# Kernel optimization log

Measured on AMD Instinct MI355X. Metric: run time of the kernel, lower is better.

## Reference

```python
import jax, jax.numpy as jnp
import numpy as np

EPS = 1e-5

def _point_batch_norm(x, gamma, beta):
    # BatchNorm1d over channel dim of (B, N, C): stats over (B, N), biased var (training mode)
    mu = jnp.mean(x, axis=(0, 1))
    var = jnp.var(x, axis=(0, 1))
    return (x - mu) * jax.lax.rsqrt(var + EPS) * gamma + beta

def setup_inputs() -> dict:
    key = jax.random.key(0)
    ks = jax.random.split(key, 10)
    B, M, N, K = 4, 16384, 32768, 16
    C, Cs, O = 64, 64, 64
    curr_coords = jax.random.normal(ks[0], (B, M, 3), jnp.float32)
    curr_feat = jax.random.normal(ks[1], (B, M, C), jnp.float32)
    skip_coords = jax.random.normal(ks[2], (B, N, 3), jnp.float32)
    skip_feat = jax.random.normal(ks[3], (B, N, Cs), jnp.float32)
    upsampling_idxs = jax.random.randint(ks[4], (B, N, K), 0, M, jnp.int64)
    s1 = 1.0 / np.sqrt(C)
    s2 = 1.0 / np.sqrt(Cs)
    W1 = jax.random.uniform(ks[5], (C, O), jnp.float32, -s1, s1)
    b1 = jax.random.uniform(ks[6], (O,), jnp.float32, -s1, s1)
    W2 = jax.random.uniform(ks[7], (Cs, O), jnp.float32, -s2, s2)
    b2 = jax.random.uniform(ks[8], (O,), jnp.float32, -s2, s2)
    g1 = jnp.ones((O,), jnp.float32); beta1 = jnp.zeros((O,), jnp.float32)
    g2 = jnp.ones((O,), jnp.float32); beta2 = jnp.zeros((O,), jnp.float32)
    return {
        "curr_coords": curr_coords, "curr_feat": curr_feat,
        "skip_coords": skip_coords, "skip_feat": skip_feat,
        "upsampling_idxs": upsampling_idxs,
        "W1": W1, "b1": b1, "g1": g1, "beta1": beta1,
        "W2": W2, "b2": b2, "g2": g2, "beta2": beta2,
    }

def reference(curr_coords, curr_feat, skip_coords, skip_feat, upsampling_idxs,
              W1, b1, g1, beta1, W2, b2, g2, beta2):
    # Gather K-NN neighbor features per skip point: (B, N, K, C), then max over K
    gathered = jax.vmap(lambda f, i: f[i])(curr_feat, upsampling_idxs)
    pooled = jnp.max(gathered, axis=2)  # (B, N, C)
    # proj: Linear -> PointBatchNorm -> ReLU
    h = jax.nn.relu(_point_batch_norm(pooled @ W1 + b1, g1, beta1))
    # proj_skip on skip features
    hs = jax.nn.relu(_point_batch_norm(skip_feat @ W2 + b2, g2, beta2))
    return jnp.concatenate([skip_coords, h, hs], axis=-1)  # (B, N, 3 + 2*O)
```

## Files before the change

### kernel.cpp

```cpp
#include <hip/hip_runtime.h>
#include <hip/hip_bf16.h>

#define BB 4
#define MM 16384
#define NN 32768
#define KK 16
#define ROWS (BB * NN)
#define OUTW 131
#define RPW 32
#define A_BLOCKS (ROWS / (RPW * 4))

__global__ __launch_bounds__(256) void k_pool_proj(
    const float* __restrict__ cf, const int* __restrict__ idxs,
    const float* __restrict__ scoord,
    const float* __restrict__ W1, const float* __restrict__ b1,
    float* __restrict__ out, float* __restrict__ acc)
{
    __shared__ float pool[4][64];
    __shared__ float lsum[64], lsq[64];
    const int lane = threadIdx.x & 63;
    const int wv   = threadIdx.x >> 6;
    if (threadIdx.x < 64) { lsum[threadIdx.x] = 0.f; lsq[threadIdx.x] = 0.f; }
    __syncthreads();

    const int xcd   = blockIdx.x & 7;
    const int batch = xcd >> 1;
    const int blkIB = ((blockIdx.x >> 3) << 1) | (xcd & 1);
    const int gw    = blkIB * 4 + wv;
    const int rbase = (batch << 15) + gw * RPW;

    float w[64];
#pragma unroll
    for (int c = 0; c < 64; ++c) w[c] = W1[c * 64 + lane];
    const float bias = b1[lane];

    float psum = 0.f, psq = 0.f;
    for (int r0 = 0; r0 < RPW; ++r0) {
        const int r = rbase + r0;
        int mi = 0;
        if (lane < KK) mi = idxs[r * KK + lane];
        float pmax = -3.402823466e38f;
#pragma unroll
        for (int k = 0; k < KK; ++k) {
            const int m = __shfl(mi, k);
            pmax = fmaxf(pmax, cf[(((batch << 14) + m) << 6) + lane]);
        }
        pool[wv][lane] = pmax;
        __builtin_amdgcn_wave_barrier();

        const float4* t4 = (const float4*)(&pool[wv][0]);
        float y = bias;
#pragma unroll
        for (int c4 = 0; c4 < 16; ++c4) {
            const float4 p = t4[c4];
            y = fmaf(p.x, w[c4 * 4 + 0], y);
            y = fmaf(p.y, w[c4 * 4 + 1], y);
            y = fmaf(p.z, w[c4 * 4 + 2], y);
            y = fmaf(p.w, w[c4 * 4 + 3], y);
        }
        __builtin_amdgcn_wave_barrier();

        const size_t ob = (size_t)r * OUTW;
        out[ob + 3 + lane] = y;
        if (lane < 3) out[ob + lane] = scoord[r * 3 + lane];
        psum += y; psq += y * y;
    }
    atomicAdd(&lsum[lane], psum);
    atomicAdd(&lsq[lane], psq);
    __syncthreads();
    if (threadIdx.x < 64) {
        atomicAdd(&acc[threadIdx.x],      lsum[threadIdx.x]);
        atomicAdd(&acc[64 + threadIdx.x], lsq[threadIdx.x]);
    }
}

__global__ __launch_bounds__(256) void k_skip_proj(
    const float* __restrict__ sf,
    const float* __restrict__ W2, const float* __restrict__ b2,
    float* __restrict__ out, float* __restrict__ acc)
{
    __shared__ float srow[4][64];
    __shared__ float lsum[64], lsq[64];
    const int lane = threadIdx.x & 63;
    const int wv   = threadIdx.x >> 6;
    if (threadIdx.x < 64) { lsum[threadIdx.x] = 0.f; lsq[threadIdx.x] = 0.f; }
    __syncthreads();

    float w[64];
#pragma unroll
    for (int c = 0; c < 64; ++c) w[c] = W2[c * 64 + lane];
    const float bias = b2[lane];

    float psum = 0.f, psq = 0.f;
    const int gw = blockIdx.x * 4 + wv;
    for (int r0 = 0; r0 < RPW; ++r0) {
        const int r = gw * RPW + r0;
        srow[wv][lane] = sf[(size_t)r * 64 + lane];
        __builtin_amdgcn_wave_barrier();

        const float4* t4 = (const float4*)(&srow[wv][0]);
        float y = bias;
#pragma unroll
        for (int c4 = 0; c4 < 16; ++c4) {
            const float4 p = t4[c4];
            y = fmaf(p.x, w[c4 * 4 + 0], y);
            y = fmaf(p.y, w[c4 * 4 + 1], y);
            y = fmaf(p.z, w[c4 * 4 + 2], y);
            y = fmaf(p.w, w[c4 * 4 + 3], y);
        }
        __builtin_amdgcn_wave_barrier();

        out[(size_t)r * OUTW + 67 + lane] = y;
        psum += y; psq += y * y;
    }
    atomicAdd(&lsum[lane], psum);
    atomicAdd(&lsq[lane], psq);
    __syncthreads();
    if (threadIdx.x < 64) {
        atomicAdd(&acc[128 + threadIdx.x], lsum[threadIdx.x]);
        atomicAdd(&acc[192 + threadIdx.x], lsq[threadIdx.x]);
    }
}

__global__ void k_stats(float* __restrict__ ws,
                        const float* __restrict__ g1, const float* __restrict__ be1,
                        const float* __restrict__ g2, const float* __restrict__ be2)
{
    const int o = threadIdx.x;
    const float inv = 1.0f / (float)ROWS;
    float m1 = ws[o] * inv;
    float v1 = ws[64 + o] * inv - m1 * m1;
    float a1 = g1[o] * rsqrtf(v1 + 1e-5f);
    ws[256 + o] = a1;
    ws[384 + o] = be1[o] - m1 * a1;
    float m2 = ws[128 + o] * inv;
    float v2 = ws[192 + o] * inv - m2 * m2;
    float a2 = g2[o] * rsqrtf(v2 + 1e-5f);
    ws[256 + 64 + o] = a2;
    ws[384 + 64 + o] = be2[o] - m2 * a2;
}

__global__ __launch_bounds__(256) void k_finalize(float* __restrict__ out,
                                                  const float* __restrict__ ws)
{
    const size_t T  = (size_t)gridDim.x * blockDim.x;
    const size_t t0 = (size_t)blockIdx.x * blockDim.x + threadIdx.x;
#pragma unroll
    for (int i = 0; i < 4; ++i) {
        const size_t e = t0 + (size_t)i * T;
        const size_t r = e >> 7;
        const int    j = (int)(e & 127);
        const size_t ad = r * OUTW + 3 + j;
        const float v = out[ad];
        out[ad] = fmaxf(fmaf(v, ws[256 + j], ws[384 + j]), 0.f);
    }
}

extern "C" void kernel_launch(void* const* d_in, const int* in_sizes, int n_in,
                              void* d_out, int out_size, void* d_ws, size_t ws_size,
                              hipStream_t stream)
{
    const float* cf     = (const float*)d_in[1];
    const float* scoord = (const float*)d_in[2];
    const float* sf     = (const float*)d_in[3];
    const int*   idxs   = (const int*)  d_in[4];
    const float* W1     = (const float*)d_in[5];
    const float* b1     = (const float*)d_in[6];
    const float* g1     = (const float*)d_in[7];
    const float* be1    = (const float*)d_in[8];
    const float* W2     = (const float*)d_in[9];
    const float* b2     = (const float*)d_in[10];
    const float* g2     = (const float*)d_in[11];
    const float* be2    = (const float*)d_in[12];
    float* out = (float*)d_out;
    float* ws  = (float*)d_ws;

    hipMemsetAsync(ws, 0, 256 * sizeof(float), stream);
    k_pool_proj<<<A_BLOCKS, 256, 0, stream>>>(cf, idxs, scoord, W1, b1, out, ws);
    k_skip_proj<<<A_BLOCKS, 256, 0, stream>>>(sf, W2, b2, out, ws);
    k_stats<<<1, 64, 0, stream>>>(ws, g1, be1, g2, be2);
    k_finalize<<<16384, 256, 0, stream>>>(out, ws);
}
```

Measured before the change: 293.2 us.

## Process four rows per iteration with batched gathers and slotted stat atomics

Both projection kernels now handle four rows per loop iteration. The pool kernel issues 64 independent gather loads per iteration to raise memory-level parallelism, and the skip kernel loads four rows with a single float4 load. Rows per wave drop to 16, which doubles the block count, and launch bounds request 5 blocks per CU. Global stat atomics are spread across 16 slots that k_stats then reduces, which cuts atomic contention. The costs are more register pressure from four accumulators and a larger workspace memset.

```diff
diff --git a/kernel.cpp b/kernel.cpp
--- a/kernel.cpp
+++ b/kernel.cpp
@@ -7,16 +7,19 @@
 #define KK 16
 #define ROWS (BB * NN)
 #define OUTW 131
-#define RPW 32
+#define RPW 16
 #define A_BLOCKS (ROWS / (RPW * 4))
-
-__global__ __launch_bounds__(256) void k_pool_proj(
+#define NSLOT 16
+#define NEG_INF -3.402823466e38f
+
+
+__global__ __launch_bounds__(256, 5) void k_pool_proj(
     const float* __restrict__ cf, const int* __restrict__ idxs,
     const float* __restrict__ scoord,
     const float* __restrict__ W1, const float* __restrict__ b1,
     float* __restrict__ out, float* __restrict__ acc)
 {
-    __shared__ float pool[4][64];
+    __shared__ float pool[4][4][64];
     __shared__ float lsum[64], lsq[64];
     const int lane = threadIdx.x & 63;
     const int wv   = threadIdx.x >> 6;
@@ -28,6 +31,7 @@
     const int blkIB = ((blockIdx.x >> 3) << 1) | (xcd & 1);
     const int gw    = blkIB * 4 + wv;
     const int rbase = (batch << 15) + gw * RPW;
+    const float* __restrict__ cfb = cf + ((size_t)batch << 20);
 
     float w[64];
 #pragma unroll
@@ -35,51 +39,76 @@
     const float bias = b1[lane];
 
     float psum = 0.f, psq = 0.f;
-    for (int r0 = 0; r0 < RPW; ++r0) {
-        const int r = rbase + r0;
-        int mi = 0;
-        if (lane < KK) mi = idxs[r * KK + lane];
-        float pmax = -3.402823466e38f;
+#pragma unroll 1
+    for (int it = 0; it < RPW / 4; ++it) {
+        const int r4 = rbase + it * 4;
+        const int mi = idxs[r4 * KK + lane];
+        float pm0 = NEG_INF, pm1 = NEG_INF, pm2 = NEG_INF, pm3 = NEG_INF;
 #pragma unroll
         for (int k = 0; k < KK; ++k) {
-            const int m = __shfl(mi, k);
-            pmax = fmaxf(pmax, cf[(((batch << 14) + m) << 6) + lane]);
-        }
-        pool[wv][lane] = pmax;
-        __builtin_amdgcn_wave_barrier();
-
-        const float4* t4 = (const float4*)(&pool[wv][0]);
-        float y = bias;
+            const int m0 = __shfl(mi, k);
+            const int m1 = __shfl(mi, 16 + k);
+            const int m2 = __shfl(mi, 32 + k);
+            const int m3 = __shfl(mi, 48 + k);
+            pm0 = fmaxf(pm0, cfb[((size_t)m0 << 6) + lane]);
+            pm1 = fmaxf(pm1, cfb[((size_t)m1 << 6) + lane]);
+            pm2 = fmaxf(pm2, cfb[((size_t)m2 << 6) + lane]);
+            pm3 = fmaxf(pm3, cfb[((size_t)m3 << 6) + lane]);
+        }
+        pool[wv][0][lane] = pm0;
+        pool[wv][1][lane] = pm1;
+        pool[wv][2][lane] = pm2;
+        pool[wv][3][lane] = pm3;
+        __builtin_amdgcn_wave_barrier();
+
+        const float4* t0 = (const float4*)&pool[wv][0][0];
+        const float4* t1 = (const float4*)&pool[wv][1][0];
+        const float4* t2 = (const float4*)&pool[wv][2][0];
+        const float4* t3 = (const float4*)&pool[wv][3][0];
+        float yy0 = bias, yy1 = bias, yy2 = bias, yy3 = bias;
 #pragma unroll
         for (int c4 = 0; c4 < 16; ++c4) {
-            const float4 p = t4[c4];
-            y = fmaf(p.x, w[c4 * 4 + 0], y);
-            y = fmaf(p.y, w[c4 * 4 + 1], y);
-            y = fmaf(p.z, w[c4 * 4 + 2], y);
-            y = fmaf(p.w, w[c4 * 4 + 3], y);
-        }
-        __builtin_amdgcn_wave_barrier();
-
-        const size_t ob = (size_t)r * OUTW;
-        out[ob + 3 + lane] = y;
-        if (lane < 3) out[ob + lane] = scoord[r * 3 + lane];
-        psum += y; psq += y * y;
+            const float4 p0 = t0[c4], p1 = t1[c4], p2 = t2[c4], p3 = t3[c4];
+            const float w0 = w[4*c4+0], w1v = w[4*c4+1], w2v = w[4*c4+2], w3v = w[4*c4+3];
+            yy0 = fmaf(p0.x, w0, yy0); yy0 = fmaf(p0.y, w1v, yy0);
+            yy0 = fmaf(p0.z, w2v, yy0); yy0 = fmaf(p0.w, w3v, yy0);
+            yy1 = fmaf(p1.x, w0, yy1); yy1 = fmaf(p1.y, w1v, yy1);
+            yy1 = fmaf(p1.z, w2v, yy1); yy1 = fmaf(p1.w, w3v, yy1);
+            yy2 = fmaf(p2.x, w0, yy2); yy2 = fmaf(p2.y, w1v, yy2);
+            yy2 = fmaf(p2.z, w2v, yy2); yy2 = fmaf(p2.w, w3v, yy2);
+            yy3 = fmaf(p3.x, w0, yy3); yy3 = fmaf(p3.y, w1v, yy3);
+            yy3 = fmaf(p3.z, w2v, yy3); yy3 = fmaf(p3.w, w3v, yy3);
+        }
+        __builtin_amdgcn_wave_barrier();
+
+        out[(size_t)(r4 + 0) * OUTW + 3 + lane] = yy0;
+        out[(size_t)(r4 + 1) * OUTW + 3 + lane] = yy1;
+        out[(size_t)(r4 + 2) * OUTW + 3 + lane] = yy2;
+        out[(size_t)(r4 + 3) * OUTW + 3 + lane] = yy3;
+        if (lane < 3) {
+#pragma unroll
+            for (int ri = 0; ri < 4; ++ri)
+                out[(size_t)(r4 + ri) * OUTW + lane] = scoord[(r4 + ri) * 3 + lane];
+        }
+        psum += yy0 + yy1 + yy2 + yy3;
+        psq  += yy0*yy0 + yy1*yy1 + yy2*yy2 + yy3*yy3;
     }
     atomicAdd(&lsum[lane], psum);
     atomicAdd(&lsq[lane], psq);
     __syncthreads();
     if (threadIdx.x < 64) {
-        atomicAdd(&acc[threadIdx.x],      lsum[threadIdx.x]);
-        atomicAdd(&acc[64 + threadIdx.x], lsq[threadIdx.x]);
-    }
-}
-
-__global__ __launch_bounds__(256) void k_skip_proj(
+        float* slot = acc + (blockIdx.x & (NSLOT - 1)) * 256;
+        atomicAdd(&slot[threadIdx.x],      lsum[threadIdx.x]);
+        atomicAdd(&slot[64 + threadIdx.x], lsq[threadIdx.x]);
+    }
+}
+
+__global__ __launch_bounds__(256, 5) void k_skip_proj(
     const float* __restrict__ sf,
     const float* __restrict__ W2, const float* __restrict__ b2,
     float* __restrict__ out, float* __restrict__ acc)
 {
-    __shared__ float srow[4][64];
+    __shared__ float tile[4][4][64];
     __shared__ float lsum[64], lsq[64];
     const int lane = threadIdx.x & 63;
     const int wv   = threadIdx.x >> 6;
@@ -90,35 +119,53 @@
 #pragma unroll
     for (int c = 0; c < 64; ++c) w[c] = W2[c * 64 + lane];
     const float bias = b2[lane];
+    const float4* __restrict__ sf4 = (const float4*)sf;
+
+    const int gw    = blockIdx.x * 4 + wv;
+    const int rbase = gw * RPW;
 
     float psum = 0.f, psq = 0.f;
-    const int gw = blockIdx.x * 4 + wv;
-    for (int r0 = 0; r0 < RPW; ++r0) {
-        const int r = gw * RPW + r0;
-        srow[wv][lane] = sf[(size_t)r * 64 + lane];
-        __builtin_amdgcn_wave_barrier();
-
-        const float4* t4 = (const float4*)(&srow[wv][0]);
-        float y = bias;
+#pragma unroll 1
+    for (int it = 0; it < RPW / 4; ++it) {
+        const int r4 = rbase + it * 4;
+        const float4 v = sf4[r4 * 16 + lane];
+        ((float4*)&tile[wv][0][0])[lane] = v;
+        __builtin_amdgcn_wave_barrier();
+
+        const float4* t0 = (const float4*)&tile[wv][0][0];
+        const float4* t1 = (const float4*)&tile[wv][1][0];
+        const float4* t2 = (const float4*)&tile[wv][2][0];
+        const float4* t3 = (const float4*)&tile[wv][3][0];
+        float yy0 = bias, yy1 = bias, yy2 = bias, yy3 = bias;
 #pragma unroll
         for (int c4 = 0; c4 < 16; ++c4) {
-            const float4 p = t4[c4];
-            y = fmaf(p.x, w[c4 * 4 + 0], y);
-            y = fmaf(p.y, w[c4 * 4 + 1], y);
-            y = fmaf(p.z, w[c4 * 4 + 2], y);
-            y = fmaf(p.w, w[c4 * 4 + 3], y);
-        }
-        __builtin_amdgcn_wave_barrier();
-
-        out[(size_t)r * OUTW + 67 + lane] = y;
-        psum += y; psq += y * y;
+            const float4 p0 = t0[c4], p1 = t1[c4], p2 = t2[c4], p3 = t3[c4];
+            const float w0 = w[4*c4+0], w1v = w[4*c4+1], w2v = w[4*c4+2], w3v = w[4*c4+3];
+            yy0 = fmaf(p0.x, w0, yy0); yy0 = fmaf(p0.y, w1v, yy0);
+            yy0 = fmaf(p0.z, w2v, yy0); yy0 = fmaf(p0.w, w3v, yy0);
+            yy1 = fmaf(p1.x, w0, yy1); yy1 = fmaf(p1.y, w1v, yy1);
+            yy1 = fmaf(p1.z, w2v, yy1); yy1 = fmaf(p1.w, w3v, yy1);
+            yy2 = fmaf(p2.x, w0, yy2); yy2 = fmaf(p2.y, w1v, yy2);
+            yy2 = fmaf(p2.z, w2v, yy2); yy2 = fmaf(p2.w, w3v, yy2);
+            yy3 = fmaf(p3.x, w0, yy3); yy3 = fmaf(p3.y, w1v, yy3);
+            yy3 = fmaf(p3.z, w2v, yy3); yy3 = fmaf(p3.w, w3v, yy3);
+        }
+        __builtin_amdgcn_wave_barrier();
+
+        out[(size_t)(r4 + 0) * OUTW + 67 + lane] = yy0;
+        out[(size_t)(r4 + 1) * OUTW + 67 + lane] = yy1;
+        out[(size_t)(r4 + 2) * OUTW + 67 + lane] = yy2;
+        out[(size_t)(r4 + 3) * OUTW + 67 + lane] = yy3;
+        psum += yy0 + yy1 + yy2 + yy3;
+        psq  += yy0*yy0 + yy1*yy1 + yy2*yy2 + yy3*yy3;
     }
     atomicAdd(&lsum[lane], psum);
     atomicAdd(&lsq[lane], psq);
     __syncthreads();
     if (threadIdx.x < 64) {
-        atomicAdd(&acc[128 + threadIdx.x], lsum[threadIdx.x]);
-        atomicAdd(&acc[192 + threadIdx.x], lsq[threadIdx.x]);
+        float* slot = acc + (blockIdx.x & (NSLOT - 1)) * 256;
+        atomicAdd(&slot[128 + threadIdx.x], lsum[threadIdx.x]);
+        atomicAdd(&slot[192 + threadIdx.x], lsq[threadIdx.x]);
     }
 }
 
@@ -127,17 +174,23 @@
                         const float* __restrict__ g2, const float* __restrict__ be2)
 {
     const int o = threadIdx.x;
+    float s1 = 0.f, q1 = 0.f, s2 = 0.f, q2 = 0.f;
+#pragma unroll
+    for (int s = 0; s < NSLOT; ++s) {
+        const float* p = ws + s * 256;
+        s1 += p[o]; q1 += p[64 + o]; s2 += p[128 + o]; q2 += p[192 + o];
+    }
     const float inv = 1.0f / (float)ROWS;
-    float m1 = ws[o] * inv;
-    float v1 = ws[64 + o] * inv - m1 * m1;
-    float a1 = g1[o] * rsqrtf(v1 + 1e-5f);
-    ws[256 + o] = a1;
-    ws[384 + o] = be1[o] - m1 * a1;
-    float m2 = ws[128 + o] * inv;
-    float v2 = ws[192 + o] * inv - m2 * m2;
-    float a2 = g2[o] * rsqrtf(v2 + 1e-5f);
-    ws[256 + 64 + o] = a2;
-    ws[384 + 64 + o] = be2[o] - m2 * a2;
+    const float m1 = s1 * inv;
+    const float v1 = q1 * inv - m1 * m1;
+    const float a1 = g1[o] * rsqrtf(v1 + 1e-5f);
+    ws[4096 + o] = a1;
+    ws[4224 + o] = be1[o] - m1 * a1;
+    const float m2 = s2 * inv;
+    const float v2 = q2 * inv - m2 * m2;
+    const float a2 = g2[o] * rsqrtf(v2 + 1e-5f);
+    ws[4096 + 64 + o] = a2;
+    ws[4224 + 64 + o] = be2[o] - m2 * a2;
 }
 
 __global__ __launch_bounds__(256) void k_finalize(float* __restrict__ out,
@@ -152,7 +205,7 @@
         const int    j = (int)(e & 127);
         const size_t ad = r * OUTW + 3 + j;
         const float v = out[ad];
-        out[ad] = fmaxf(fmaf(v, ws[256 + j], ws[384 + j]), 0.f);
+        out[ad] = fmaxf(fmaf(v, ws[4096 + j], ws[4224 + j]), 0.f);
     }
 }
 
@@ -175,7 +228,7 @@
     float* out = (float*)d_out;
     float* ws  = (float*)d_ws;
 
-    hipMemsetAsync(ws, 0, 256 * sizeof(float), stream);
+    hipMemsetAsync(ws, 0, NSLOT * 256 * sizeof(float), stream);
     k_pool_proj<<<A_BLOCKS, 256, 0, stream>>>(cf, idxs, scoord, W1, b1, out, ws);
     k_skip_proj<<<A_BLOCKS, 256, 0, stream>>>(sf, W2, b2, out, ws);
     k_stats<<<1, 64, 0, stream>>>(ws, g1, be1, g2, be2);
```

Measured after the change: 677.7 us. 131% more time.
